# Kernel optimization log

Measured on AMD Instinct MI355X. Metric: run time of the kernel, lower is better.

Reference implementation:

```python
import jax, jax.numpy as jnp
import numpy as np

B, C, W, H = 8, 256, 64, 64
C8 = C // 8


def setup_inputs() -> dict:
    key = jax.random.key(0)
    ks = jax.random.split(key, 8)
    # xavier_uniform for 1x1 convs: bound = sqrt(6/(fan_in+fan_out))
    def xavier(k, out_c, in_c):
        bound = np.sqrt(6.0 / (in_c + out_c))
        return jax.random.uniform(k, (out_c, in_c), jnp.float32, -bound, bound)
    return {
        "x": jax.random.normal(ks[0], (B, C, W, H), jnp.float32),
        "Wf": xavier(ks[1], C8, C),
        "bf": jnp.zeros((C8,), jnp.float32),
        "Wg": xavier(ks[2], C8, C),
        "bg": jnp.zeros((C8,), jnp.float32),
        "Wh": xavier(ks[3], C, C),
        "bh": jnp.zeros((C,), jnp.float32),
        "gamma": jnp.zeros((1,), jnp.float32),
    }


def reference(x, Wf, bf, Wg, bg, Wh, bh, gamma):
    b, c, w, h = x.shape
    n = w * h
    xf = x.reshape(b, c, n)                                   # (B, C, N)
    # 1x1 convs == per-position channel GEMMs
    f = jnp.einsum('oc,bcn->bon', Wf, xf) + bf[None, :, None]  # (B, C/8, N)
    g = jnp.einsum('oc,bcn->bon', Wg, xf) + bg[None, :, None]  # (B, C/8, N)
    hh = jnp.einsum('oc,bcn->bon', Wh, xf) + bh[None, :, None] # (B, C, N)
    # attention[b,i,j] = softmax_j( f[b,:,i] . g[b,:,j] )
    att = jax.nn.softmax(jnp.einsum('boi,boj->bij', f, g), axis=-1)
    # torch.bmm(h, attention): out[b,c,i] = sum_k h[b,c,k] * att[b,k,i]
    sa = jnp.einsum('bck,bki->bci', hh, att).reshape(b, c, w, h)
    return gamma * sa + x
```

## Files before the change

kernel.cpp:

```cpp
#include <hip/hip_runtime.h>
#include <hip/hip_bf16.h>

#define BB 8
#define CC 256
#define NN 4096
#define LOG2E 1.44269504088896340736f
#define SHIFT 48.0f

typedef __attribute__((ext_vector_type(8))) short short8;
typedef __attribute__((ext_vector_type(4))) float f32x4;

static __device__ __forceinline__ unsigned short f2b(float x) {
  __hip_bfloat16 h = __float2bfloat16(x);
  return *reinterpret_cast<unsigned short*>(&h);
}
static __device__ __forceinline__ unsigned int pk2(float a, float b) {
  return (unsigned int)f2b(a) | ((unsigned int)f2b(b) << 16);
}


__global__ __launch_bounds__(256) void k_wprep(
    const float* __restrict__ Wf, const float* __restrict__ bfv,
    const float* __restrict__ Wg, const float* __restrict__ bgv,
    const float* __restrict__ Wh, const float* __restrict__ bhv,
    unsigned short* __restrict__ wA, float* __restrict__ ball)
{
  const int t = threadIdx.x;
  const int fi = blockIdx.x * 4 + (t >> 6);
  const int l = t & 63;
  const int mg = fi >> 3, kg = fi & 7;
  const int o = mg * 16 + (l & 15);
  const int c0 = kg * 32 + (l >> 4) * 8;
  const float* src; float scale = 1.0f;
  if (o < 32)      { src = Wf + (size_t)o * CC; scale = LOG2E; }
  else if (o < 64) { src = Wg + (size_t)(o - 32) * CC; }
  else             { src = Wh + (size_t)(o - 64) * CC; }
  float4 a = *(const float4*)(src + c0);
  float4 c = *(const float4*)(src + c0 + 4);
  short8 v;
  v[0] = (short)f2b(a.x * scale); v[1] = (short)f2b(a.y * scale);
  v[2] = (short)f2b(a.z * scale); v[3] = (short)f2b(a.w * scale);
  v[4] = (short)f2b(c.x * scale); v[5] = (short)f2b(c.y * scale);
  v[6] = (short)f2b(c.z * scale); v[7] = (short)f2b(c.w * scale);
  *(short8*)(wA + (size_t)fi * 512 + l * 8) = v;
  if (blockIdx.x == 0 && t < 320)
    ball[t] = (t < 32) ? bfv[t] * LOG2E : (t < 64) ? bgv[t - 32] : bhv[t - 64];
}

__global__ __launch_bounds__(512) void k_fgh(
    const float* __restrict__ x, const unsigned short* __restrict__ wA,
    const float* __restrict__ ball,
    unsigned short* __restrict__ fA, unsigned short* __restrict__ gB,
    unsigned short* __restrict__ hA)
{
  __shared__ __align__(16) char smem[41984];
  unsigned short* xb = (unsigned short*)smem;
  unsigned short* TL = (unsigned short*)smem;
  const int bid = blockIdx.x;
  const int b = bid & 7, i0 = (bid >> 3) * 64;
  const int t = threadIdx.x, w = t >> 6, l = t & 63;
  const int ig_w = w & 3, mg0 = (w >> 2) * 10;
  f32x4 acc[10] = {};
  for (int cc = 0; cc < 4; ++cc) {
    __syncthreads();
    {
      short8 v;
      const float* xp = x + ((size_t)b * CC + cc * 64 + w * 8) * NN + i0 + l;
      #pragma unroll
      for (int e = 0; e < 8; ++e) v[e] = (short)f2b(xp[(size_t)e * NN]);
      int frag = (w >> 2) * 4 + (l >> 4);
      int lp = (w & 3) * 16 + (l & 15);
      *(short8*)(xb + (frag * 64 + lp) * 8) = v;
    }
    __syncthreads();
    #pragma unroll
    for (int kg2 = 0; kg2 < 2; ++kg2) {
      short8 bfrag = *(const short8*)(xb + ((kg2 * 4 + ig_w) * 64 + l) * 8);
      int kg = cc * 2 + kg2;
      #pragma unroll
      for (int j = 0; j < 10; ++j) {
        short8 afrag = *(const short8*)(wA +
            ((size_t)((mg0 + j) * 8 + kg)) * 512 + l * 8);
        acc[j] = __builtin_amdgcn_mfma_f32_16x16x32_bf16(afrag, bfrag, acc[j], 0, 0, 0);
      }
    }
  }
  __syncthreads();
  #pragma unroll
  for (int j = 0; j < 10; ++j) {
    int ob = (mg0 + j) * 16 + (l >> 4) * 4;
    float4 bl = *(const float4*)(ball + ob);
    int irow = ig_w * 16 + (l & 15);
    ushort4 pv;
    pv.x = f2b(acc[j][0] + bl.x); pv.y = f2b(acc[j][1] + bl.y);
    pv.z = f2b(acc[j][2] + bl.z); pv.w = f2b(acc[j][3] + bl.w);
    *(ushort4*)(TL + irow * 328 + ob) = pv;
  }
  __syncthreads();
  if (t < 256) {
    int kg_p = t >> 6;
    int o8 = (l >> 4) * 8;
    int irow = kg_p * 16 + (l & 15);
    short8 vf = *(const short8*)(TL + irow * 328 + o8);
    short8 vg = *(const short8*)(TL + irow * 328 + 32 + o8);
    size_t kgG = (size_t)b * 256 + (i0 >> 4) + kg_p;
    *(short8*)(fA + kgG * 512 + l * 8) = vf;
    *(short8*)(gB + kgG * 512 + l * 8) = vg;
  }
  #pragma unroll
  for (int q = 0; q < 4; ++q) {
    int slot = t + q * 512;
    int fr = slot >> 6, ll = slot & 63;
    int cg = fr >> 1, kcl = fr & 1;
    int orow = 64 + cg * 16 + (ll & 15);
    int pbase = kcl * 32 + (ll >> 4) * 8;
    short8 v;
    #pragma unroll
    for (int e = 0; e < 8; ++e) v[e] = (short)TL[(pbase + e) * 328 + orow];
    size_t idx = (((size_t)b * 16 + cg) * 128 + (i0 >> 5) + kcl) * 512 + ll * 8;
    *(short8*)(hA + idx) = v;
  }
}

__global__ __launch_bounds__(256, 4) void k_stats(
    const unsigned short* __restrict__ fA, const unsigned short* __restrict__ gB,
    float* __restrict__ cshift)
{
  const int bid = blockIdx.x;
  const int b = bid & 7, kt = bid >> 3;
  const int t = threadIdx.x, w = t >> 6, l = t & 63;
  const int li = l & 15, lh = l >> 4;
  short8 af = *(const short8*)(fA + ((size_t)b * 256 + kt * 4 + w) * 512 + l * 8);
  const unsigned short* gb = gB + (size_t)b * 256 * 512 + l * 8;
  f32x4 zero = {0.f, 0.f, 0.f, 0.f};
  float s[4] = {0.f, 0.f, 0.f, 0.f};
  short8 bc[4], bn[4];
  #pragma unroll
  for (int jj = 0; jj < 4; ++jj)
    bc[jj] = *(const short8*)(gb + (size_t)jj * 512);
  for (int j4 = 0; j4 < 64; ++j4) {
    const int jn = (j4 < 63) ? (j4 + 1) : 63;
    #pragma unroll
    for (int jj = 0; jj < 4; ++jj)
      bn[jj] = *(const short8*)(gb + (size_t)(jn * 4 + jj) * 512);
    #pragma unroll
    for (int jj = 0; jj < 4; ++jj) {
      f32x4 d = __builtin_amdgcn_mfma_f32_16x16x32_bf16(af, bc[jj], zero, 0, 0, 0);
      s[0] += exp2f(d[0] - SHIFT);
      s[1] += exp2f(d[1] - SHIFT);
      s[2] += exp2f(d[2] - SHIFT);
      s[3] += exp2f(d[3] - SHIFT);
    }
    #pragma unroll
    for (int jj = 0; jj < 4; ++jj) bc[jj] = bn[jj];
  }
  #pragma unroll
  for (int mk = 1; mk < 16; mk <<= 1)
    #pragma unroll
    for (int r = 0; r < 4; ++r) s[r] += __shfl_xor(s[r], mk);
  if (li == 0) {
    #pragma unroll
    for (int r = 0; r < 4; ++r) {
      size_t idx = (size_t)b * NN + kt * 64 + w * 16 + lh * 4 + r;
      cshift[idx] = SHIFT + log2f(fmaxf(s[r], 1e-30f));
    }
  }
}

__global__ __launch_bounds__(512, 4) void k_out(
    const unsigned short* __restrict__ fA, const unsigned short* __restrict__ gB,
    const unsigned short* __restrict__ hA,
    const float* __restrict__ csv,
    const float* __restrict__ x, const float* __restrict__ gamma,
    float* __restrict__ out)
{
  __shared__ __align__(16) unsigned short pbuf[2 * 16 * 512];
  const int bid = blockIdx.x;
  const int b = bid & 7, i0 = (bid >> 3) * 64;
  const int t = threadIdx.x, w = t >> 6, l = t & 63;
  const int li = l & 15, lh = l >> 4;
  const unsigned short* fAb = fA + ((size_t)b * 256 + w) * 512 + l * 8;
  const unsigned short* hAb = hA + ((size_t)b * 16 + w * 2) * (size_t)128 * 512 + l * 8;
  const float* cs = csv + (size_t)b * NN + w * 16 + lh * 4;
  short8 g[4];
  #pragma unroll
  for (int ig = 0; ig < 4; ++ig)
    g[ig] = *(const short8*)(gB + ((size_t)b * 256 + (i0 >> 4) + ig) * 512 + l * 8);
  const int pl = ((w & 1) * 2 + (lh >> 1)) * 16 + li;
  const int pwo = pl * 8 + (lh & 1) * 4;
  f32x4 zero = {0.f, 0.f, 0.f, 0.f};
  f32x4 acc[2][4] = {};
  for (int ch = 0; ch < 32; ++ch) {
    short8 hf[8];
    #pragma unroll
    for (int cg = 0; cg < 2; ++cg)
      #pragma unroll
      for (int kb = 0; kb < 4; ++kb)
        hf[cg * 4 + kb] = *(const short8*)(hAb +
            ((size_t)cg * 128 + ch * 4 + kb) * 512);
    short8 af = *(const short8*)(fAb + (size_t)ch * 8 * 512);
    float4 cc = *(const float4*)(cs + ch * 128);
    unsigned short* pb = pbuf + (ch & 1) * (16 * 512);
    #pragma unroll
    for (int ig = 0; ig < 4; ++ig) {
      f32x4 sfr = __builtin_amdgcn_mfma_f32_16x16x32_bf16(af, g[ig], zero, 0, 0, 0);
      uint2 v;
      v.x = pk2(exp2f(sfr[0] - cc.x), exp2f(sfr[1] - cc.y));
      v.y = pk2(exp2f(sfr[2] - cc.z), exp2f(sfr[3] - cc.w));
      *(uint2*)(pb + ((size_t)((w >> 1) * 4 + ig)) * 512 + pwo) = v;
    }
    __syncthreads();
    #pragma unroll
    for (int kb = 0; kb < 4; ++kb)
      #pragma unroll
      for (int ig = 0; ig < 4; ++ig) {
        short8 pf = *(const short8*)(pb + ((kb * 4 + ig) * 64 + l) * 8);
        acc[0][ig] = __builtin_amdgcn_mfma_f32_16x16x32_bf16(pf, hf[kb], acc[0][ig], 0, 0, 0);
        acc[1][ig] = __builtin_amdgcn_mfma_f32_16x16x32_bf16(pf, hf[4 + kb], acc[1][ig], 0, 0, 0);
      }
  }
  const float gm = gamma[0];
  #pragma unroll
  for (int cg = 0; cg < 2; ++cg)
    #pragma unroll
    for (int ig = 0; ig < 4; ++ig) {
      int c = w * 32 + cg * 16 + li;
      int i = i0 + ig * 16 + lh * 4;
      size_t off = ((size_t)b * CC + c) * NN + i;
      float4 xv = *(const float4*)(x + off);
      float4 ov;
      ov.x = gm * acc[cg][ig][0] + xv.x;
      ov.y = gm * acc[cg][ig][1] + xv.y;
      ov.z = gm * acc[cg][ig][2] + xv.z;
      ov.w = gm * acc[cg][ig][3] + xv.w;
      *(float4*)(out + off) = ov;
    }
}

extern "C" void kernel_launch(void* const* d_in, const int* in_sizes, int n_in,
                              void* d_out, int out_size, void* d_ws, size_t ws_size,
                              hipStream_t stream)
{
  const float* x     = (const float*)d_in[0];
  const float* Wf    = (const float*)d_in[1];
  const float* bf    = (const float*)d_in[2];
  const float* Wg    = (const float*)d_in[3];
  const float* bg    = (const float*)d_in[4];
  const float* Wh    = (const float*)d_in[5];
  const float* bh    = (const float*)d_in[6];
  const float* gamma = (const float*)d_in[7];
  float* out = (float*)d_out;

  char* wsb = (char*)d_ws;
  float* cshift = (float*)(wsb + 131072);
  unsigned short* wA = (unsigned short*)(wsb + 262144);
  float* ball        = (float*)(wsb + 425984);
  unsigned short* fA = (unsigned short*)(wsb + 427520);
  unsigned short* gB = (unsigned short*)(wsb + 2524672);
  unsigned short* hA = (unsigned short*)(wsb + 4621824);

  k_wprep<<<40,  256, 0, stream>>>(Wf, bf, Wg, bg, Wh, bh, wA, ball);
  k_fgh  <<<512, 512, 0, stream>>>(x, wA, ball, fA, gB, hA);
  k_stats<<<512, 256, 0, stream>>>(fA, gB, cshift);
  k_out  <<<512, 512, 0, stream>>>(fA, gB, hA, cshift, x, gamma, out);
}
```

Before: 160.0 us.

## Stage g tiles through LDS in stats and software-pipeline P generation in output kernel

k_stats now runs 512-thread blocks that cooperatively load each 16-fragment g tile into double-buffered LDS. Before, every wave read all of g from global memory on its own. The grid is halved, and each block covers 128 query rows instead of 64. In k_out, the exp/pack of the next chunk's P tile is computed before the MFMA accumulation of the current chunk, so that work overlaps with the matrix ops and only one barrier is needed per iteration; s_setprio also raises priority around the MFMA block. The costs are extra LDS use, more barriers in k_stats, and higher register pressure from the prefetched operands.

Measured after the change: 165.2 us. 3.3% more time.

```diff
diff --git a/kernel.cpp b/kernel.cpp
--- a/kernel.cpp
+++ b/kernel.cpp
@@ -122,37 +122,45 @@
   }
 }
 
-__global__ __launch_bounds__(256, 4) void k_stats(
+__global__ __launch_bounds__(512) void k_stats(
     const unsigned short* __restrict__ fA, const unsigned short* __restrict__ gB,
     float* __restrict__ cshift)
 {
+  __shared__ __align__(16) unsigned short sg[2][16 * 512];
   const int bid = blockIdx.x;
   const int b = bid & 7, kt = bid >> 3;
   const int t = threadIdx.x, w = t >> 6, l = t & 63;
   const int li = l & 15, lh = l >> 4;
-  short8 af = *(const short8*)(fA + ((size_t)b * 256 + kt * 4 + w) * 512 + l * 8);
-  const unsigned short* gb = gB + (size_t)b * 256 * 512 + l * 8;
+  short8 af = *(const short8*)(fA + ((size_t)b * 256 + kt * 8 + w) * 512 + l * 8);
+  const unsigned short* gb = gB + (size_t)b * 256 * 512;
   f32x4 zero = {0.f, 0.f, 0.f, 0.f};
+  {
+    uint4 v0 = *(const uint4*)(gb + ((size_t)(w * 2 + 0) * 64 + l) * 8);
+    uint4 v1 = *(const uint4*)(gb + ((size_t)(w * 2 + 1) * 64 + l) * 8);
+    *(uint4*)(&sg[0][((w * 2 + 0) * 64 + l) * 8]) = v0;
+    *(uint4*)(&sg[0][((w * 2 + 1) * 64 + l) * 8]) = v1;
+  }
+  __syncthreads();
   float s[4] = {0.f, 0.f, 0.f, 0.f};
-  short8 bc[4], bn[4];
-  #pragma unroll
-  for (int jj = 0; jj < 4; ++jj)
-    bc[jj] = *(const short8*)(gb + (size_t)jj * 512);
-  for (int j4 = 0; j4 < 64; ++j4) {
-    const int jn = (j4 < 63) ? (j4 + 1) : 63;
-    #pragma unroll
-    for (int jj = 0; jj < 4; ++jj)
-      bn[jj] = *(const short8*)(gb + (size_t)(jn * 4 + jj) * 512);
-    #pragma unroll
-    for (int jj = 0; jj < 4; ++jj) {
-      f32x4 d = __builtin_amdgcn_mfma_f32_16x16x32_bf16(af, bc[jj], zero, 0, 0, 0);
+  for (int jt = 0; jt < 16; ++jt) {
+    if (jt < 15) {
+      uint4 v0 = *(const uint4*)(gb + ((size_t)((jt + 1) * 16 + w * 2 + 0) * 64 + l) * 8);
+      uint4 v1 = *(const uint4*)(gb + ((size_t)((jt + 1) * 16 + w * 2 + 1) * 64 + l) * 8);
+      unsigned short* dst = &sg[(jt + 1) & 1][0];
+      *(uint4*)(dst + ((w * 2 + 0) * 64 + l) * 8) = v0;
+      *(uint4*)(dst + ((w * 2 + 1) * 64 + l) * 8) = v1;
+    }
+    const unsigned short* src = &sg[jt & 1][0];
+    #pragma unroll
+    for (int jf = 0; jf < 16; ++jf) {
+      short8 bfrag = *(const short8*)(src + (jf * 64 + l) * 8);
+      f32x4 d = __builtin_amdgcn_mfma_f32_16x16x32_bf16(af, bfrag, zero, 0, 0, 0);
       s[0] += exp2f(d[0] - SHIFT);
       s[1] += exp2f(d[1] - SHIFT);
       s[2] += exp2f(d[2] - SHIFT);
       s[3] += exp2f(d[3] - SHIFT);
     }
-    #pragma unroll
-    for (int jj = 0; jj < 4; ++jj) bc[jj] = bn[jj];
+    __syncthreads();
   }
   #pragma unroll
   for (int mk = 1; mk < 16; mk <<= 1)
@@ -161,7 +169,7 @@
   if (li == 0) {
     #pragma unroll
     for (int r = 0; r < 4; ++r) {
-      size_t idx = (size_t)b * NN + kt * 64 + w * 16 + lh * 4 + r;
+      size_t idx = (size_t)b * NN + (kt * 8 + w) * 16 + lh * 4 + r;
       cshift[idx] = SHIFT + log2f(fmaxf(s[r], 1e-30f));
     }
   }
@@ -190,7 +198,22 @@
   const int pwo = pl * 8 + (lh & 1) * 4;
   f32x4 zero = {0.f, 0.f, 0.f, 0.f};
   f32x4 acc[2][4] = {};
+  short8 afc = *(const short8*)(fAb);
+  float4 ccc = *(const float4*)(cs);
+  #pragma unroll
+  for (int ig = 0; ig < 4; ++ig) {
+    f32x4 sfr = __builtin_amdgcn_mfma_f32_16x16x32_bf16(afc, g[ig], zero, 0, 0, 0);
+    uint2 v;
+    v.x = pk2(exp2f(sfr[0] - ccc.x), exp2f(sfr[1] - ccc.y));
+    v.y = pk2(exp2f(sfr[2] - ccc.z), exp2f(sfr[3] - ccc.w));
+    *(uint2*)(pbuf + ((size_t)((w >> 1) * 4 + ig)) * 512 + pwo) = v;
+  }
+  afc = *(const short8*)(fAb + (size_t)8 * 512);
+  ccc = *(const float4*)(cs + 128);
+  __syncthreads();
   for (int ch = 0; ch < 32; ++ch) {
+    unsigned short* pb  = pbuf + (ch & 1) * (16 * 512);
+    unsigned short* pnx = pbuf + ((ch + 1) & 1) * (16 * 512);
     short8 hf[8];
     #pragma unroll
     for (int cg = 0; cg < 2; ++cg)
@@ -198,18 +221,20 @@
       for (int kb = 0; kb < 4; ++kb)
         hf[cg * 4 + kb] = *(const short8*)(hAb +
             ((size_t)cg * 128 + ch * 4 + kb) * 512);
-    short8 af = *(const short8*)(fAb + (size_t)ch * 8 * 512);
-    float4 cc = *(const float4*)(cs + ch * 128);
-    unsigned short* pb = pbuf + (ch & 1) * (16 * 512);
-    #pragma unroll
-    for (int ig = 0; ig < 4; ++ig) {
-      f32x4 sfr = __builtin_amdgcn_mfma_f32_16x16x32_bf16(af, g[ig], zero, 0, 0, 0);
-      uint2 v;
-      v.x = pk2(exp2f(sfr[0] - cc.x), exp2f(sfr[1] - cc.y));
-      v.y = pk2(exp2f(sfr[2] - cc.z), exp2f(sfr[3] - cc.w));
-      *(uint2*)(pb + ((size_t)((w >> 1) * 4 + ig)) * 512 + pwo) = v;
-    }
-    __syncthreads();
+    if (ch < 31) {
+      #pragma unroll
+      for (int ig = 0; ig < 4; ++ig) {
+        f32x4 sfr = __builtin_amdgcn_mfma_f32_16x16x32_bf16(afc, g[ig], zero, 0, 0, 0);
+        uint2 v;
+        v.x = pk2(exp2f(sfr[0] - ccc.x), exp2f(sfr[1] - ccc.y));
+        v.y = pk2(exp2f(sfr[2] - ccc.z), exp2f(sfr[3] - ccc.w));
+        *(uint2*)(pnx + ((size_t)((w >> 1) * 4 + ig)) * 512 + pwo) = v;
+      }
+      const int ch2 = (ch < 30) ? (ch + 2) : 31;
+      afc = *(const short8*)(fAb + (size_t)ch2 * 8 * 512);
+      ccc = *(const float4*)(cs + ch2 * 128);
+    }
+    __builtin_amdgcn_s_setprio(1);
     #pragma unroll
     for (int kb = 0; kb < 4; ++kb)
       #pragma unroll
@@ -218,6 +243,8 @@
         acc[0][ig] = __builtin_amdgcn_mfma_f32_16x16x32_bf16(pf, hf[kb], acc[0][ig], 0, 0, 0);
         acc[1][ig] = __builtin_amdgcn_mfma_f32_16x16x32_bf16(pf, hf[4 + kb], acc[1][ig], 0, 0, 0);
       }
+    __builtin_amdgcn_s_setprio(0);
+    __syncthreads();
   }
   const float gm = gamma[0];
   #pragma unroll
@@ -261,6 +288,6 @@
 
   k_wprep<<<40,  256, 0, stream>>>(Wf, bf, Wg, bg, Wh, bh, wA, ball);
   k_fgh  <<<512, 512, 0, stream>>>(x, wA, ball, fA, gB, hA);
-  k_stats<<<512, 256, 0, stream>>>(fA, gB, cshift);
+  k_stats<<<256, 512, 0, stream>>>(fA, gB, cshift);
   k_out  <<<512, 512, 0, stream>>>(fA, gB, hA, cshift, x, gamma, out);
 }
```
